# Optimization experiments

Measured on AMD Instinct MI355X. Metric: run time of the kernel, lower is better.

## Reference

```python
import jax, jax.numpy as jnp
import numpy as np
from functools import partial

U, I, D, E = 8192, 8192, 128, 524288
N = U + I


def setup_inputs() -> dict:
    key = jax.random.key(0)
    ks = jax.random.split(key, 12)
    s = 1.0 / np.sqrt(D)
    return {
        "user_emb": jax.random.normal(ks[0], (U, D), jnp.float32) * 0.1,
        "item_emb": jax.random.normal(ks[1], (I, D), jnp.float32) * 0.1,
        "adj_rows": jax.random.randint(ks[2], (E,), 0, N, jnp.int32),
        "adj_cols": jax.random.randint(ks[3], (E,), 0, N, jnp.int32),
        "adj_vals": jax.random.uniform(ks[4], (E,), jnp.float32) * (1.0 / 32.0),
        "wq": jax.random.normal(ks[5], (D, D), jnp.float32) * s,
        "bq": jnp.zeros((D,), jnp.float32),
        "wk": jax.random.normal(ks[6], (D, D), jnp.float32) * s,
        "bk": jnp.zeros((D,), jnp.float32),
        "wv": jax.random.normal(ks[7], (D, D), jnp.float32) * s,
        "bv": jnp.zeros((D,), jnp.float32),
        "fw": jax.random.normal(ks[8], (D, D), jnp.float32) * s,
        "fb": jnp.zeros((D,), jnp.float32),
        "n_layers": 3,
        "topk": 32,
    }


def _spmm(vals, rows, cols, x):
    # sparse [N,N] @ dense [N,D] via gather + segment_sum
    return jax.ops.segment_sum(vals[:, None] * x[cols], rows, num_segments=N)


def reference(user_emb, item_emb, adj_rows, adj_cols, adj_vals,
              wq, bq, wk, bk, wv, bv, fw, fb, n_layers, topk):
    ego = jnp.concatenate([user_emb, item_emb], axis=0)  # [N, D]
    layers = []
    for _ in range(n_layers):
        ego = _spmm(adj_vals, adj_rows, adj_cols, ego)
        layers.append(ego)
    all_emb = jnp.mean(jnp.stack(layers, axis=1), axis=1)  # [N, D]

    # full similarity + topk + gather
    sim = ego @ ego.T                                # [N, N]
    idx = jax.lax.top_k(sim, topk)[1]                # [N, K]
    samples = jnp.take(ego, idx, axis=0)             # [N, K, D]

    # per-node small attention over the K samples (dropout = eval identity)
    q = ego @ wq.T + bq                              # [N, D]
    k_ = samples @ wk.T + bk                         # [N, K, D]
    v = samples @ wv.T + bv                          # [N, K, D]
    scores = jnp.einsum('nd,nkd->nk', q, k_) / jnp.sqrt(jnp.float32(D))
    attn = jax.nn.softmax(scores, axis=-1)
    atten_embed = jnp.einsum('nk,nkd->nd', attn, v) + 0.1 * ego

    # fusion gating (softmax over dim=1, i.e. the node axis, as in source)
    a1 = jnp.tanh(all_emb @ fw.T + fb)
    a2 = jnp.tanh(atten_embed @ fw.T + fb)
    a = jax.nn.softmax(jnp.stack([a1, a2], axis=0), axis=1)  # [2, N, D]
    fusion = a[0] * all_emb + a[1] * atten_embed

    return (all_emb[:U], all_emb[U:],
            atten_embed[:U], atten_embed[U:],
            fusion[:U], fusion[U:])
```

## Files before the change

### kernel.cpp

```cpp
#include <hip/hip_runtime.h>
#include <math.h>

#define U_ 8192
#define I_ 8192
#define D_ 128
#define E_ 524288
#define N_ 16384
#define K_ 32
#define CAP_ 512

typedef unsigned short u16;
typedef unsigned int u32;
typedef unsigned long long u64;
typedef __attribute__((ext_vector_type(8))) short bf16x8;
typedef __attribute__((ext_vector_type(4))) float f32x4;

__global__ void k_init(const float* __restrict__ wq, const float* __restrict__ wk,
                       const float* __restrict__ bq, const float* __restrict__ wv,
                       const float* __restrict__ fw,
                       float* __restrict__ M, float* __restrict__ bqk,
                       float* __restrict__ wvT, float* __restrict__ fwdT,
                       int* __restrict__ cnt, float* __restrict__ cs1,
                       float* __restrict__ cs2,
                       float* __restrict__ svec, int* __restrict__ gcount,
                       int* __restrict__ failn) {
  const int tid = blockIdx.x * 256 + threadIdx.x;
  cnt[tid] = 0;
  gcount[tid] = 0;
  if (tid < 2048) { cs1[tid] = 0.f; cs2[tid] = 0.f; }
  if (tid < 128) svec[tid] = 0.f;
  if (tid == 0) *failn = 0;
  const int i = tid >> 7, j = tid & 127;
  float s = 0.f;
  for (int l = 0; l < 128; ++l) s += wq[l * 128 + i] * wk[l * 128 + j];
  M[tid] = s;
  wvT[i * 128 + j] = wv[j * 128 + i];
  fwdT[i * 128 + j] = fw[j * 128 + i];
  if (tid < 128) {
    float s2 = 0.f;
    for (int l = 0; l < 128; ++l) s2 += bq[l] * wk[l * 128 + tid];
    bqk[tid] = s2;
  }
}

__global__ void k_concat(const float* __restrict__ user, const float* __restrict__ item,
                         float* __restrict__ ego,
                         const int* __restrict__ rows, int* __restrict__ cnt) {
  const int i = blockIdx.x * 256 + threadIdx.x;
  ego[i] = (i < U_ * D_) ? user[i] : item[i - U_ * D_];
  if (i < E_) atomicAdd(&cnt[rows[i]], 1);
}

__global__ void k_scan(const int* __restrict__ cnt, int* __restrict__ row_ptr,
                       int* __restrict__ cursor) {
  __shared__ int wsum[16];
  __shared__ int carry_s;
  const int t = threadIdx.x;
  const int lane = t & 63, wid = t >> 6;
  if (t == 0) carry_s = 0;
  __syncthreads();
  for (int c = 0; c < N_ / 1024; ++c) {
    const int x = cnt[c * 1024 + t];
    int incl = x;
#pragma unroll
    for (int off = 1; off < 64; off <<= 1) {
      const int v = __shfl_up(incl, off, 64);
      if (lane >= off) incl += v;
    }
    if (lane == 63) wsum[wid] = incl;
    __syncthreads();
    if (wid == 0) {
      int s = (lane < 16) ? wsum[lane] : 0;
#pragma unroll
      for (int off = 1; off < 16; off <<= 1) {
        const int v = __shfl_up(s, off, 64);
        if (lane >= off) s += v;
      }
      if (lane < 16) wsum[lane] = s;
    }
    __syncthreads();
    const int carry = carry_s;
    const int wbase = wid ? wsum[wid - 1] : 0;
    const int excl = carry + wbase + incl - x;
    row_ptr[c * 1024 + t] = excl;
    cursor[c * 1024 + t] = excl;
    __syncthreads();
    if (t == 1023) carry_s += wsum[15];
    __syncthreads();
  }
  if (t == 0) row_ptr[N_] = carry_s;
}

__global__ void k_scatter(const int* __restrict__ rows, const int* __restrict__ cols,
                          const float* __restrict__ vals, int* __restrict__ cursor,
                          int* __restrict__ ccol, float* __restrict__ cval) {
  const int e = blockIdx.x * 256 + threadIdx.x;
  const int r = rows[e];
  const int p = atomicAdd(&cursor[r], 1);
  ccol[p] = cols[e];
  cval[p] = vals[e];
}

__global__ __launch_bounds__(128) void k_spmm(const float* __restrict__ x,
                                              float* __restrict__ y,
                                              float* __restrict__ sum,
                                              const int* __restrict__ row_ptr,
                                              const int* __restrict__ ccol,
                                              const float* __restrict__ cval,
                                              const int first, const int last) {
  const int r = blockIdx.x, d = threadIdx.x;
  const int b = row_ptr[r], e = row_ptr[r + 1];
  double a[8];
#pragma unroll
  for (int u = 0; u < 8; ++u) a[u] = 0.0;
  int i = b;
  for (; i + 7 < e; i += 8) {
#pragma unroll
    for (int u = 0; u < 8; ++u)
      a[u] += (double)cval[i + u] * (double)x[ccol[i + u] * 128 + d];
  }
  for (; i < e; ++i)
    a[0] += (double)cval[i] * (double)x[ccol[i] * 128 + d];
  const float f = (float)((((a[0] + a[1]) + (a[2] + a[3])) + ((a[4] + a[5]) + (a[6] + a[7]))));
  y[r * 128 + d] = f;
  float s = first ? f : sum[r * 128 + d] + f;
  if (last) s = s / 3.0f;
  sum[r * 128 + d] = s;
}

__global__ __launch_bounds__(256) void k_split_t(const float* __restrict__ x,
                                                 u16* __restrict__ Gh, u16* __restrict__ Gl,
                                                 u16* __restrict__ XTh, u16* __restrict__ XTl,
                                                 float* __restrict__ svec) {
  __shared__ u16 lh[128 * 66];
  __shared__ u16 ll[128 * 66];
  const int tid = threadIdx.x;
  const int r0 = blockIdx.x * 64;
  float colsum = 0.f;
  for (int s = 0; s < 32; ++s) {
    const int idx = tid + s * 256;
    const int r = idx >> 7, d = idx & 127;
    const float v = x[(r0 + r) * 128 + d];
    colsum += v;
    unsigned int u = __float_as_uint(v);
    u += 0x7fffu + ((u >> 16) & 1u);
    const u16 h = (u16)(u >> 16);
    const float hf = __uint_as_float(((unsigned int)h) << 16);
    const float l = v - hf;
    unsigned int u2 = __float_as_uint(l);
    u2 += 0x7fffu + ((u2 >> 16) & 1u);
    const u16 lo = (u16)(u2 >> 16);
    Gh[(r0 + r) * 128 + d] = h;
    Gl[(r0 + r) * 128 + d] = lo;
    lh[d * 66 + r] = h;
    ll[d * 66 + r] = lo;
  }
  atomicAdd(&svec[tid & 127], colsum);
  __syncthreads();
  for (int s = 0; s < 32; ++s) {
    const int idx = tid + s * 256;
    const int d = idx >> 6, rr = idx & 63;
    XTh[d * 16384 + r0 + rr] = lh[d * 66 + rr];
    XTl[d * 16384 + r0 + rr] = ll[d * 66 + rr];
  }
}

__global__ __launch_bounds__(256) void k_c2mfma(const u16* __restrict__ XTh,
                                                const u16* __restrict__ XTl,
                                                float* __restrict__ C2part) {
  const int tid = threadIdx.x, w = tid >> 6, lane = tid & 63;
  const int n16 = lane & 15, kq = lane >> 4;
  const int c0 = blockIdx.x * 64;
  f32x4 acc[2][8];
#pragma unroll
  for (int a = 0; a < 2; ++a)
#pragma unroll
    for (int b = 0; b < 8; ++b) acc[a][b] = (f32x4){0.f, 0.f, 0.f, 0.f};
  for (int ks = 0; ks < 2; ++ks) {
    const int c = c0 + ks * 32 + kq * 8;
    bf16x8 Fh[8], Fl[8];
#pragma unroll
    for (int g = 0; g < 8; ++g) {
      const int base = (g * 16 + n16) * 16384 + c;
      Fh[g] = *(const bf16x8*)&XTh[base];
      Fl[g] = *(const bf16x8*)&XTl[base];
    }
#pragma unroll
    for (int a = 0; a < 2; ++a) {
      const int tr = w * 2 + a;
#pragma unroll
      for (int b = 0; b < 8; ++b) {
        acc[a][b] = __builtin_amdgcn_mfma_f32_16x16x32_bf16(Fl[tr], Fh[b], acc[a][b], 0, 0, 0);
        acc[a][b] = __builtin_amdgcn_mfma_f32_16x16x32_bf16(Fh[tr], Fl[b], acc[a][b], 0, 0, 0);
        acc[a][b] = __builtin_amdgcn_mfma_f32_16x16x32_bf16(Fh[tr], Fh[b], acc[a][b], 0, 0, 0);
      }
    }
  }
  float* dst = C2part + (size_t)blockIdx.x * 16384;
#pragma unroll
  for (int a = 0; a < 2; ++a) {
    const int tr = w * 2 + a;
#pragma unroll
    for (int b = 0; b < 8; ++b)
#pragma unroll
      for (int i = 0; i < 4; ++i)
        dst[(tr * 16 + kq * 4 + i) * 128 + b * 16 + n16] = acc[a][b][i];
  }
}

__global__ void k_c2red(const float* __restrict__ C2part, float* __restrict__ C2) {
  const int e = blockIdx.x * 256 + threadIdx.x;
  float s = 0.f;
  for (int b = 0; b < 256; ++b) s += C2part[(size_t)b * 16384 + e];
  C2[e] = s;
}

__global__ __launch_bounds__(128) void k_tau(const float* __restrict__ x,
                                             const float* __restrict__ C2,
                                             const float* __restrict__ svec,
                                             float* __restrict__ tau) {
  __shared__ float xs[8][128];
  __shared__ double r1[8][2], r2[8][2];
  const int tid = threadIdx.x;
  const int lane = tid & 63, wid = tid >> 6;
  const int n0 = blockIdx.x * 8;
#pragma unroll
  for (int rr = 0; rr < 8; ++rr) xs[rr][tid] = x[(n0 + rr) * 128 + tid];
  __syncthreads();
  double y[8];
#pragma unroll
  for (int rr = 0; rr < 8; ++rr) y[rr] = 0.0;
  for (int k2 = 0; k2 < 128; ++k2) {
    const double c = (double)C2[k2 * 128 + tid];
#pragma unroll
    for (int rr = 0; rr < 8; ++rr) y[rr] += (double)xs[rr][k2] * c;
  }
  const double sv = (double)svec[tid];
#pragma unroll
  for (int rr = 0; rr < 8; ++rr) {
    double v1 = (double)xs[rr][tid] * y[rr];
    double v2 = (double)xs[rr][tid] * sv;
#pragma unroll
    for (int off = 32; off; off >>= 1) {
      v1 += __shfl_xor(v1, off, 64);
      v2 += __shfl_xor(v2, off, 64);
    }
    if (lane == 0) { r1[rr][wid] = v1; r2[rr][wid] = v2; }
  }
  __syncthreads();
  if (tid < 8) {
    const double exy = (r1[tid][0] + r1[tid][1]) / 16384.0;
    const double m = (r2[tid][0] + r2[tid][1]) / 16384.0;
    double var = exy - m * m;
    if (var < 0.0) var = 0.0;
    tau[n0 + tid] = (float)(m + 2.55 * sqrt(var));
  }
}

__global__ __launch_bounds__(256) void k_qk(const float* __restrict__ ego,
                                            const float* __restrict__ M,
                                            const float* __restrict__ bqk,
                                            float* __restrict__ qkout) {
  __shared__ float xs[8][128];
  const int tid = threadIdx.x;
  const int r0 = blockIdx.x * 8;
#pragma unroll
  for (int s = 0; s < 4; ++s) {
    const int idx = tid + s * 256;
    xs[idx >> 7][idx & 127] = ego[r0 * 128 + idx];
  }
  __syncthreads();
  const int j = tid & 127, h = tid >> 7;
  const float bj = bqk[j];
  float acc[4];
#pragma unroll
  for (int r = 0; r < 4; ++r) acc[r] = bj;
  for (int d = 0; d < 128; d += 4) {
    const float w0 = M[(d + 0) * 128 + j];
    const float w1 = M[(d + 1) * 128 + j];
    const float w2 = M[(d + 2) * 128 + j];
    const float w3 = M[(d + 3) * 128 + j];
#pragma unroll
    for (int r = 0; r < 4; ++r) {
      const float4 xv = *(const float4*)&xs[h * 4 + r][d];
      acc[r] += xv.x * w0 + xv.y * w1 + xv.z * w2 + xv.w * w3;
    }
  }
#pragma unroll
  for (int r = 0; r < 4; ++r)
    qkout[(r0 + h * 4 + r) * 128 + j] = acc[r];
}

__device__ __forceinline__ void gload_lds16(const u16* g, u16* l) {
  __builtin_amdgcn_global_load_lds(
      (const __attribute__((address_space(1))) void*)g,
      (__attribute__((address_space(3))) void*)l, 16, 0, 0);
}

__global__ __launch_bounds__(256) void k_simmfma(const u16* __restrict__ Gh,
                                                 const u16* __restrict__ Gl,
                                                 const float* __restrict__ tau,
                                                 int* __restrict__ gstripcnt,
                                                 int2* __restrict__ gbuf) {
  __shared__ __align__(16) u16 lh[64 * 128];
  __shared__ int cnt128[128];
  const int tid = threadIdx.x;
  const int w = tid >> 6, lane = tid & 63;
  const int strip = blockIdx.x & 15, rgrp = blockIdx.x >> 4;
  const int n16 = lane & 15, kq = lane >> 4;

  if (tid < 128) cnt128[tid] = 0;

  const int rowbase = rgrp * 128 + w * 32;
  bf16x8 Bh[2][4], Bl[2][4];
#pragma unroll
  for (int rg = 0; rg < 2; ++rg) {
    const int row = rowbase + rg * 16 + n16;
#pragma unroll
    for (int q = 0; q < 4; ++q) {
      Bh[rg][q] = *(const bf16x8*)&Gh[row * 128 + q * 32 + kq * 8];
      Bl[rg][q] = *(const bf16x8*)&Gl[row * 128 + q * 32 + kq * 8];
    }
  }
  const float tau0 = tau[rowbase + n16];
  const float tau1 = tau[rowbase + 16 + n16];
  const int col0 = strip * 1024;

  for (int st = 0; st < 16; ++st) {
    const int cb = col0 + st * 64;
    __syncthreads();
#pragma unroll
    for (int ii = 0; ii < 4; ++ii) {
      const int srow = w * 16 + ii * 4 + kq;
      const int chunk = n16 ^ (srow & 7);
      gload_lds16(Gh + (((size_t)(cb + srow)) << 7) + chunk * 8,
                  lh + ((w * 16 + ii * 4) << 7));
    }
    __syncthreads();
#pragma unroll
    for (int ct = 0; ct < 4; ++ct) {
      const int ar = ct * 16 + n16;
      const char* lbase = (const char*)lh + ar * 256;
      bf16x8 Ah[4];
#pragma unroll
      for (int q = 0; q < 4; ++q)
        Ah[q] = *(const bf16x8*)(lbase + ((q * 64 + kq * 16) ^ ((ar & 7) << 4)));
#pragma unroll
      for (int rg = 0; rg < 2; ++rg) {
        f32x4 p = {0.f, 0.f, 0.f, 0.f};
        f32x4 r = {0.f, 0.f, 0.f, 0.f};
#pragma unroll
        for (int q = 0; q < 4; ++q) {
          p = __builtin_amdgcn_mfma_f32_16x16x32_bf16(Ah[q], Bh[rg][q], p, 0, 0, 0);
          r = __builtin_amdgcn_mfma_f32_16x16x32_bf16(Ah[q], Bl[rg][q], r, 0, 0, 0);
        }
        const float tv = rg ? tau1 : tau0;
        const int lrow = w * 32 + rg * 16 + n16;
        const int row = rgrp * 128 + lrow;
#pragma unroll
        for (int i = 0; i < 4; ++i) {
          const float v = p[i] + r[i];
          if (v > tv) {
            const int c = cb + ct * 16 + kq * 4 + i;
            const int pos = atomicAdd(&cnt128[lrow], 1);
            if (pos < 32)
              gbuf[row * CAP_ + strip * 32 + pos] = make_int2(c, __float_as_int(v));
          }
        }
      }
    }
  }
  __syncthreads();
  if (tid < 128) gstripcnt[(rgrp * 128 + tid) * 16 + strip] = cnt128[tid];
}

__global__ __launch_bounds__(256) void k_refine(const int* __restrict__ gstripcnt,
                                                const int2* __restrict__ gbuf,
                                                int* __restrict__ topk_idx,
                                                int* __restrict__ failq,
                                                int* __restrict__ failn) {
  __shared__ u64 lk[4][CAP_];
  const int tid = threadIdx.x, w = tid >> 6, lane = tid & 63;
  const int n = blockIdx.x * 4 + w;

  const int scn = (lane < 16) ? gstripcnt[n * 16 + lane] : 0;
  int total = 0, over = 0;
#pragma unroll
  for (int s = 0; s < 16; ++s) {
    const int c = __shfl(scn, s, 64);
    total += c;
    over |= (c > 32);
  }
  const int bad = (total < 36 || total > CAP_ || over);
  const int cnt = bad ? 0 : total;

  int base = 0;
#pragma unroll
  for (int s = 0; s < 16; ++s) {
    const int c = __shfl(scn, s, 64);
    if (!bad && lane < c) {
      const int2 p = gbuf[n * CAP_ + s * 32 + lane];
      u32 uv = (u32)p.y;
      uv = (uv >> 31) ? ~uv : (uv | 0x80000000u);
      lk[w][base + lane] = ((u64)uv << 32) | (u64)(16383 - p.x);
    }
    base += bad ? 0 : c;
  }
  __syncthreads();

  for (int ci = lane; ci < cnt; ci += 64) {
    const u64 kk = lk[w][ci];
    int r = 0;
#pragma unroll 4
    for (int j = 0; j < cnt; ++j)
      r += (lk[w][j] > kk) ? 1 : 0;
    if (r < 32) topk_idx[n * 32 + r] = 16383 - (int)(u32)(kk & 0xffffffffu);
  }
  if (bad) {
    if (lane == 0) {
      const int s = atomicAdd(failn, 1);
      if (s < 64) failq[s] = n;
    }
    if (lane < 32) topk_idx[n * 32 + lane] = 0;
  }
}

__global__ __launch_bounds__(256) void k_fallback(const float* __restrict__ x,
                                                  const int* __restrict__ failq,
                                                  const int* __restrict__ failn,
                                                  double* __restrict__ fsim,
                                                  int* __restrict__ topk_idx) {
  const int nf = *failn;
  const int which = blockIdx.x;
  if (which >= nf || which >= 64) return;
  const int row = failq[which];
  __shared__ float xs[128];
  __shared__ double bm[256];
  __shared__ int bc[256];
  const int tid = threadIdx.x;
  if (tid < 128) xs[tid] = x[row * 128 + tid];
  __syncthreads();
  double* fs = fsim + (size_t)which * 16384;
  for (int c = tid; c < 16384; c += 256) {
    const float4* xp = (const float4*)&x[c * 128];
    double a = 0.0;
    for (int d = 0; d < 32; ++d) {
      const float4 v = xp[d];
      a += (double)xs[d * 4 + 0] * (double)v.x + (double)xs[d * 4 + 1] * (double)v.y +
           (double)xs[d * 4 + 2] * (double)v.z + (double)xs[d * 4 + 3] * (double)v.w;
    }
    fs[c] = a;
  }
  __syncthreads();
  for (int r = 0; r < 32; ++r) {
    double m = -1.0e300; int mc = 0;
    for (int c = tid; c < 16384; c += 256) {
      const double v = fs[c];
      if (v > m || (v == m && c < mc)) { m = v; mc = c; }
    }
    bm[tid] = m; bc[tid] = mc;
    __syncthreads();
    for (int s = 128; s; s >>= 1) {
      if (tid < s) {
        if (bm[tid + s] > bm[tid] || (bm[tid + s] == bm[tid] && bc[tid + s] < bc[tid])) {
          bm[tid] = bm[tid + s]; bc[tid] = bc[tid + s];
        }
      }
      __syncthreads();
    }
    if (tid == 0) { topk_idx[row * 32 + r] = bc[0]; fs[bc[0]] = -1.0e300; }
    __syncthreads();
  }
}

__global__ __launch_bounds__(128) void k_attn(const float* __restrict__ ego,
                                              float* __restrict__ qk,
                                              const int* __restrict__ topk_idx) {
  __shared__ float qv[128];
  __shared__ float sm[32 * 129];
  __shared__ int tki[32];
  __shared__ float sc[32];
  __shared__ float psum[128];
  const int n = blockIdx.x, tid = threadIdx.x;
  qv[tid] = qk[n * 128 + tid];
  if (tid < 32) tki[tid] = topk_idx[n * 32 + tid] & 16383;
  __syncthreads();
  for (int e = tid; e < 32 * 128; e += 128) {
    const int k2 = e >> 7, d = e & 127;
    sm[k2 * 129 + d] = ego[tki[k2] * 128 + d];
  }
  __syncthreads();
  {
    const int kk = tid & 31, part = tid >> 5;
    float s = 0.f;
    const int d0 = part * 32;
    for (int d = d0; d < d0 + 32; ++d) s += qv[d] * sm[kk * 129 + d];
    psum[tid] = s;
  }
  __syncthreads();
  if (tid < 32) {
    float v = psum[tid] + psum[tid + 32] + psum[tid + 64] + psum[tid + 96];
    v *= (1.0f / 11.313708498984760f);
    float m = v;
#pragma unroll
    for (int off = 16; off; off >>= 1) m = fmaxf(m, __shfl_xor(m, off, 32));
    const float e = expf(v - m);
    float ssum = e;
#pragma unroll
    for (int off = 16; off; off >>= 1) ssum += __shfl_xor(ssum, off, 32);
    sc[tid] = e / ssum;
  }
  __syncthreads();
  float sad = 0.f;
  for (int k2 = 0; k2 < 32; ++k2) sad += sc[k2] * sm[k2 * 129 + tid];
  qk[n * 128 + tid] = sad;
}

__global__ __launch_bounds__(256) void k_attnfuse(const float* __restrict__ sa,
                                                  const float* __restrict__ ego,
                                                  const float* __restrict__ allemb,
                                                  const float* __restrict__ wvT,
                                                  const float* __restrict__ bv,
                                                  const float* __restrict__ fwdT,
                                                  const float* __restrict__ fb,
                                                  float* __restrict__ atten,
                                                  float* __restrict__ z1,
                                                  float* __restrict__ z2,
                                                  float* __restrict__ cs1,
                                                  float* __restrict__ cs2) {
  __shared__ float xs[8][128];
  __shared__ float xa[8][128];
  __shared__ float as_[8][128];
  __shared__ float red1[2][128];
  __shared__ float red2[2][128];
  const int tid = threadIdx.x;
  const int r0 = blockIdx.x * 8;
#pragma unroll
  for (int s = 0; s < 4; ++s) {
    const int idx = tid + s * 256;
    const int rr = idx >> 7, d = idx & 127;
    xs[rr][d] = sa[(r0 + rr) * 128 + d];
    xa[rr][d] = allemb[(r0 + rr) * 128 + d];
  }
  __syncthreads();
  const int j = tid & 127, h = tid >> 7;
  {
    const float bj = bv[j];
    float acc[4];
#pragma unroll
    for (int r = 0; r < 4; ++r) acc[r] = bj;
    for (int d = 0; d < 128; d += 4) {
      const float w0 = wvT[(d + 0) * 128 + j];
      const float w1 = wvT[(d + 1) * 128 + j];
      const float w2 = wvT[(d + 2) * 128 + j];
      const float w3 = wvT[(d + 3) * 128 + j];
#pragma unroll
      for (int r = 0; r < 4; ++r) {
        const float4 xv = *(const float4*)&xs[h * 4 + r][d];
        acc[r] += xv.x * w0 + xv.y * w1 + xv.z * w2 + xv.w * w3;
      }
    }
#pragma unroll
    for (int r = 0; r < 4; ++r) {
      const int n = r0 + h * 4 + r;
      const float av = acc[r] + 0.1f * ego[n * 128 + j];
      atten[n * 128 + j] = av;
      as_[h * 4 + r][j] = av;
    }
  }
  __syncthreads();
  const float fbj = fb[j];
  float acc1[4], acc2[4];
#pragma unroll
  for (int r = 0; r < 4; ++r) { acc1[r] = fbj; acc2[r] = fbj; }
  for (int d = 0; d < 128; d += 4) {
    const float w0 = fwdT[(d + 0) * 128 + j];
    const float w1 = fwdT[(d + 1) * 128 + j];
    const float w2 = fwdT[(d + 2) * 128 + j];
    const float w3 = fwdT[(d + 3) * 128 + j];
#pragma unroll
    for (int r = 0; r < 4; ++r) {
      const int rr = h * 4 + r;
      const float4 xv = *(const float4*)&xa[rr][d];
      const float4 av = *(const float4*)&as_[rr][d];
      acc1[r] += xv.x * w0 + xv.y * w1 + xv.z * w2 + xv.w * w3;
      acc2[r] += av.x * w0 + av.y * w1 + av.z * w2 + av.w * w3;
    }
  }
  float ls1 = 0.f, ls2 = 0.f;
#pragma unroll
  for (int r = 0; r < 4; ++r) {
    const int rr = h * 4 + r;
    const float t1 = tanhf(acc1[r]);
    const float t2 = tanhf(acc2[r]);
    z1[(r0 + rr) * 128 + j] = t1;
    z2[(r0 + rr) * 128 + j] = t2;
    ls1 += expf(t1 - 1.0f);
    ls2 += expf(t2 - 1.0f);
  }
  red1[h][j] = ls1;
  red2[h][j] = ls2;
  __syncthreads();
  if (h == 0) {
    const int rep = blockIdx.x & 15;
    atomicAdd(&cs1[rep * 128 + j], red1[0][j] + red1[1][j]);
    atomicAdd(&cs2[rep * 128 + j], red2[0][j] + red2[1][j]);
  }
}

__global__ void k_fuse2(const float* __restrict__ allemb, const float* __restrict__ atten,
                        const float* __restrict__ z1, const float* __restrict__ z2,
                        const float* __restrict__ cs1, const float* __restrict__ cs2,
                        float* __restrict__ fusion) {
  __shared__ float s1[128], s2[128];
  const int tid = threadIdx.x;
  if (tid < 128) {
    float a = 0.f, b = 0.f;
#pragma unroll
    for (int rep = 0; rep < 16; ++rep) {
      a += cs1[rep * 128 + tid];
      b += cs2[rep * 128 + tid];
    }
    s1[tid] = a; s2[tid] = b;
  }
  __syncthreads();
  const int i = blockIdx.x * 256 + tid;
  const int j = i & 127;
  const float a1 = expf(z1[i] - 1.0f) / s1[j];
  const float a2 = expf(z2[i] - 1.0f) / s2[j];
  fusion[i] = a1 * allemb[i] + a2 * atten[i];
}

extern "C" void kernel_launch(void* const* d_in, const int* in_sizes, int n_in,
                              void* d_out, int out_size, void* d_ws, size_t ws_size,
                              hipStream_t stream) {
  (void)in_sizes; (void)n_in; (void)out_size; (void)ws_size;
  const float* user = (const float*)d_in[0];
  const float* item = (const float*)d_in[1];
  const int* adj_rows = (const int*)d_in[2];
  const int* adj_cols = (const int*)d_in[3];
  const float* adj_vals = (const float*)d_in[4];
  const float* wq = (const float*)d_in[5];
  const float* bq = (const float*)d_in[6];
  const float* wk = (const float*)d_in[7];
  const float* wv = (const float*)d_in[9];
  const float* bv = (const float*)d_in[10];
  const float* fw = (const float*)d_in[11];
  const float* fb = (const float*)d_in[12];

  float* out = (float*)d_out;
  float* allemb = out;
  float* atten = out + (size_t)N_ * D_;
  float* fusion = out + (size_t)2 * N_ * D_;

  char* ws = (char*)d_ws;
  size_t off = 0;
  auto alloc = [&](size_t bytes) { char* p = ws + off; off += (bytes + 255) & ~(size_t)255; return p; };
  float* ego_a = (float*)alloc((size_t)N_ * D_ * 4);
  float* ego_b = (float*)alloc((size_t)N_ * D_ * 4);
  float* qkbuf = (float*)alloc((size_t)N_ * D_ * 4);
  u16* Gh = (u16*)alloc((size_t)N_ * D_ * 2);
  u16* Gl = (u16*)alloc((size_t)N_ * D_ * 2);
  u16* XTh = (u16*)alloc((size_t)N_ * D_ * 2);
  u16* XTl = (u16*)alloc((size_t)N_ * D_ * 2);
  int2* gbuf = (int2*)alloc((size_t)N_ * CAP_ * 8);
  float* z1 = (float*)gbuf;
  float* z2 = (float*)alloc((size_t)N_ * D_ * 4);
  int* topk_idx = (int*)alloc((size_t)N_ * 32 * 4);
  int* ccol = (int*)alloc((size_t)E_ * 4);
  float* cval = (float*)alloc((size_t)E_ * 4);
  int* cnt = (int*)alloc((size_t)N_ * 4);
  int* row_ptr = (int*)alloc((size_t)(N_ + 1) * 4);
  int* cursor = (int*)alloc((size_t)N_ * 4);
  float* M = (float*)alloc(128 * 128 * 4);
  float* bqk = (float*)alloc(128 * 4);
  float* wvT = (float*)alloc(128 * 128 * 4);
  float* fwdT = (float*)alloc(128 * 128 * 4);
  float* cs1 = (float*)alloc(16 * 128 * 4);
  float* cs2 = (float*)alloc(16 * 128 * 4);
  float* C2 = (float*)alloc(128 * 128 * 4);
  float* C2part = (float*)alloc((size_t)256 * 16384 * 4);
  float* svec = (float*)alloc(128 * 4);
  float* tau = (float*)alloc((size_t)N_ * 4);
  int* gcount = (int*)alloc((size_t)N_ * 4);
  int* gstripcnt = (int*)alloc((size_t)N_ * 16 * 4);
  int* failq = (int*)alloc(64 * 4);
  int* failn = (int*)alloc(4);
  double* fsim = (double*)alloc((size_t)64 * N_ * 8);

  k_init<<<64, 256, 0, stream>>>(wq, wk, bq, wv, fw, M, bqk, wvT, fwdT, cnt, cs1, cs2, svec, gcount, failn);
  k_concat<<<8192, 256, 0, stream>>>(user, item, ego_a, adj_rows, cnt);
  k_scan<<<1, 1024, 0, stream>>>(cnt, row_ptr, cursor);
  k_scatter<<<2048, 256, 0, stream>>>(adj_rows, adj_cols, adj_vals, cursor, ccol, cval);

  k_spmm<<<N_, 128, 0, stream>>>(ego_a, ego_b, allemb, row_ptr, ccol, cval, 1, 0);
  k_spmm<<<N_, 128, 0, stream>>>(ego_b, ego_a, allemb, row_ptr, ccol, cval, 0, 0);
  k_spmm<<<N_, 128, 0, stream>>>(ego_a, ego_b, allemb, row_ptr, ccol, cval, 0, 1);

  k_split_t<<<256, 256, 0, stream>>>(ego_b, Gh, Gl, XTh, XTl, svec);
  k_c2mfma<<<256, 256, 0, stream>>>(XTh, XTl, C2part);
  k_c2red<<<64, 256, 0, stream>>>(C2part, C2);
  k_tau<<<2048, 128, 0, stream>>>(ego_b, C2, svec, tau);

  k_qk<<<2048, 256, 0, stream>>>(ego_b, M, bqk, qkbuf);
  k_simmfma<<<2048, 256, 0, stream>>>(Gh, Gl, tau, gstripcnt, gbuf);
  k_refine<<<4096, 256, 0, stream>>>(gstripcnt, gbuf, topk_idx, failq, failn);
  k_fallback<<<64, 256, 0, stream>>>(ego_b, failq, failn, fsim, topk_idx);
  k_attn<<<N_, 128, 0, stream>>>(ego_b, qkbuf, topk_idx);
  k_attnfuse<<<2048, 256, 0, stream>>>(qkbuf, ego_b, allemb, wvT, bv, fwdT, fb,
                                       atten, z1, z2, cs1, cs2);
  k_fuse2<<<8192, 256, 0, stream>>>(allemb, atten, z1, z2, cs1, cs2, fusion);
}
```

Baseline: 664.8 us.

## Vectorize concat, SpMM index loads, fuse2, and widen attention block

The concat and fuse2 kernels now use float4 loads and stores with a quarter of the blocks. SpMM aligns its start index and reads column indices and values as int4/float4 pairs. The attention kernel moves to 256 threads with float2 gathers and splits the weighted sum across two halves. Together these aim to cut memory instruction count and raise per-block parallelism, at the cost of extra reductions and an alignment prologue in SpMM.

```diff
diff --git a/kernel.cpp b/kernel.cpp
--- a/kernel.cpp
+++ b/kernel.cpp
@@ -47,8 +47,10 @@
                          float* __restrict__ ego,
                          const int* __restrict__ rows, int* __restrict__ cnt) {
   const int i = blockIdx.x * 256 + threadIdx.x;
-  ego[i] = (i < U_ * D_) ? user[i] : item[i - U_ * D_];
-  if (i < E_) atomicAdd(&cnt[rows[i]], 1);
+  const float4 v = (i < U_ * D_ / 4) ? ((const float4*)user)[i]
+                                     : ((const float4*)item)[i - U_ * D_ / 4];
+  ((float4*)ego)[i] = v;
+  atomicAdd(&cnt[rows[i]], 1);
 }
 
 __global__ void k_scan(const int* __restrict__ cnt, int* __restrict__ row_ptr,
@@ -114,10 +116,21 @@
 #pragma unroll
   for (int u = 0; u < 8; ++u) a[u] = 0.0;
   int i = b;
+  for (; i < e && (i & 3); ++i)
+    a[0] += (double)cval[i] * (double)x[ccol[i] * 128 + d];
   for (; i + 7 < e; i += 8) {
-#pragma unroll
-    for (int u = 0; u < 8; ++u)
-      a[u] += (double)cval[i + u] * (double)x[ccol[i + u] * 128 + d];
+    const int4 ca = *(const int4*)&ccol[i];
+    const int4 cb = *(const int4*)&ccol[i + 4];
+    const float4 va = *(const float4*)&cval[i];
+    const float4 vb = *(const float4*)&cval[i + 4];
+    a[0] += (double)va.x * (double)x[ca.x * 128 + d];
+    a[1] += (double)va.y * (double)x[ca.y * 128 + d];
+    a[2] += (double)va.z * (double)x[ca.z * 128 + d];
+    a[3] += (double)va.w * (double)x[ca.w * 128 + d];
+    a[4] += (double)vb.x * (double)x[cb.x * 128 + d];
+    a[5] += (double)vb.y * (double)x[cb.y * 128 + d];
+    a[6] += (double)vb.z * (double)x[cb.z * 128 + d];
+    a[7] += (double)vb.w * (double)x[cb.w * 128 + d];
   }
   for (; i < e; ++i)
     a[0] += (double)cval[i] * (double)x[ccol[i] * 128 + d];
@@ -473,33 +486,36 @@
   }
 }
 
-__global__ __launch_bounds__(128) void k_attn(const float* __restrict__ ego,
+__global__ __launch_bounds__(256) void k_attn(const float* __restrict__ ego,
                                               float* __restrict__ qk,
                                               const int* __restrict__ topk_idx) {
   __shared__ float qv[128];
-  __shared__ float sm[32 * 129];
+  __shared__ float sm[32 * 130];
   __shared__ int tki[32];
   __shared__ float sc[32];
-  __shared__ float psum[128];
+  __shared__ float psum[256];
   const int n = blockIdx.x, tid = threadIdx.x;
-  qv[tid] = qk[n * 128 + tid];
+  if (tid < 128) qv[tid] = qk[n * 128 + tid];
   if (tid < 32) tki[tid] = topk_idx[n * 32 + tid] & 16383;
   __syncthreads();
-  for (int e = tid; e < 32 * 128; e += 128) {
-    const int k2 = e >> 7, d = e & 127;
-    sm[k2 * 129 + d] = ego[tki[k2] * 128 + d];
+  for (int e = tid; e < 2048; e += 256) {
+    const int k2 = e >> 6, d2 = e & 63;
+    const float2 v = *(const float2*)&ego[(size_t)tki[k2] * 128 + d2 * 2];
+    *(float2*)&sm[k2 * 130 + d2 * 2] = v;
   }
   __syncthreads();
   {
     const int kk = tid & 31, part = tid >> 5;
     float s = 0.f;
-    const int d0 = part * 32;
-    for (int d = d0; d < d0 + 32; ++d) s += qv[d] * sm[kk * 129 + d];
+    const int d0 = part * 16;
+    for (int d = d0; d < d0 + 16; ++d) s += qv[d] * sm[kk * 130 + d];
     psum[tid] = s;
   }
   __syncthreads();
   if (tid < 32) {
-    float v = psum[tid] + psum[tid + 32] + psum[tid + 64] + psum[tid + 96];
+    float v = 0.f;
+#pragma unroll
+    for (int p = 0; p < 8; ++p) v += psum[tid + p * 32];
     v *= (1.0f / 11.313708498984760f);
     float m = v;
 #pragma unroll
@@ -511,9 +527,15 @@
     sc[tid] = e / ssum;
   }
   __syncthreads();
-  float sad = 0.f;
-  for (int k2 = 0; k2 < 32; ++k2) sad += sc[k2] * sm[k2 * 129 + tid];
-  qk[n * 128 + tid] = sad;
+  {
+    const int d = tid & 127, half = tid >> 7;
+    float s = 0.f;
+    const int k0 = half * 16;
+    for (int k2 = k0; k2 < k0 + 16; ++k2) s += sc[k2] * sm[k2 * 130 + d];
+    psum[tid] = s;
+  }
+  __syncthreads();
+  if (tid < 128) qk[n * 128 + tid] = psum[tid] + psum[tid + 128];
 }
 
 __global__ __launch_bounds__(256) void k_attnfuse(const float* __restrict__ sa,
@@ -625,10 +647,17 @@
   }
   __syncthreads();
   const int i = blockIdx.x * 256 + tid;
-  const int j = i & 127;
-  const float a1 = expf(z1[i] - 1.0f) / s1[j];
-  const float a2 = expf(z2[i] - 1.0f) / s2[j];
-  fusion[i] = a1 * allemb[i] + a2 * atten[i];
+  const int j0 = (i & 31) * 4;
+  const float4 zv1 = ((const float4*)z1)[i];
+  const float4 zv2 = ((const float4*)z2)[i];
+  const float4 xv = ((const float4*)allemb)[i];
+  const float4 av = ((const float4*)atten)[i];
+  float4 o;
+  o.x = expf(zv1.x - 1.0f) / s1[j0 + 0] * xv.x + expf(zv2.x - 1.0f) / s2[j0 + 0] * av.x;
+  o.y = expf(zv1.y - 1.0f) / s1[j0 + 1] * xv.y + expf(zv2.y - 1.0f) / s2[j0 + 1] * av.y;
+  o.z = expf(zv1.z - 1.0f) / s1[j0 + 2] * xv.z + expf(zv2.z - 1.0f) / s2[j0 + 2] * av.z;
+  o.w = expf(zv1.w - 1.0f) / s1[j0 + 3] * xv.w + expf(zv2.w - 1.0f) / s2[j0 + 3] * av.w;
+  ((float4*)fusion)[i] = o;
 }
 
 extern "C" void kernel_launch(void* const* d_in, const int* in_sizes, int n_in,
@@ -689,7 +718,7 @@
   double* fsim = (double*)alloc((size_t)64 * N_ * 8);
 
   k_init<<<64, 256, 0, stream>>>(wq, wk, bq, wv, fw, M, bqk, wvT, fwdT, cnt, cs1, cs2, svec, gcount, failn);
-  k_concat<<<8192, 256, 0, stream>>>(user, item, ego_a, adj_rows, cnt);
+  k_concat<<<2048, 256, 0, stream>>>(user, item, ego_a, adj_rows, cnt);
   k_scan<<<1, 1024, 0, stream>>>(cnt, row_ptr, cursor);
   k_scatter<<<2048, 256, 0, stream>>>(adj_rows, adj_cols, adj_vals, cursor, ccol, cval);
 
@@ -706,8 +735,8 @@
   k_simmfma<<<2048, 256, 0, stream>>>(Gh, Gl, tau, gstripcnt, gbuf);
   k_refine<<<4096, 256, 0, stream>>>(gstripcnt, gbuf, topk_idx, failq, failn);
   k_fallback<<<64, 256, 0, stream>>>(ego_b, failq, failn, fsim, topk_idx);
-  k_attn<<<N_, 128, 0, stream>>>(ego_b, qkbuf, topk_idx);
+  k_attn<<<N_, 256, 0, stream>>>(ego_b, qkbuf, topk_idx);
   k_attnfuse<<<2048, 256, 0, stream>>>(qkbuf, ego_b, allemb, wvT, bv, fwdT, fb,
                                        atten, z1, z2, cs1, cs2);
-  k_fuse2<<<8192, 256, 0, stream>>>(allemb, atten, z1, z2, cs1, cs2, fusion);
-}
+  k_fuse2<<<2048, 256, 0, stream>>>(allemb, atten, z1, z2, cs1, cs2, fusion);
+}
```

Result: no change. 662.4 us (-0.4%).
